# Optimization experiments

Measured on AMD Instinct MI355X. Metric: run time of the kernel, lower is better.

## Reference

```python
import jax, jax.numpy as jnp
import numpy as np

D_MODEL = 1024
N_HEADS = 16
D_K = 64
BATCH = 2
SEQ = 2048
LN_EPS = 1e-5


def setup_inputs() -> dict:
    key = jax.random.key(0)
    ks = jax.random.split(key, 6)
    s = 1.0 / np.sqrt(D_MODEL)
    return {
        "h": jax.random.normal(ks[0], (BATCH, SEQ, D_MODEL), dtype=jnp.float32),
        "Wq": jax.random.normal(ks[1], (D_MODEL, D_MODEL), dtype=jnp.float32) * s,
        "bq": jnp.zeros((D_MODEL,), jnp.float32),
        "Wk": jax.random.normal(ks[2], (D_MODEL, D_MODEL), dtype=jnp.float32) * s,
        "bk": jnp.zeros((D_MODEL,), jnp.float32),
        "Wv": jax.random.normal(ks[3], (D_MODEL, D_MODEL), dtype=jnp.float32) * s,
        "bv": jnp.zeros((D_MODEL,), jnp.float32),
        "Wo": jax.random.normal(ks[4], (D_MODEL, D_MODEL), dtype=jnp.float32) * s,
        "bo": jnp.zeros((D_MODEL,), jnp.float32),
        "ln_w": jnp.ones((D_MODEL,), jnp.float32),
        "ln_b": jnp.zeros((D_MODEL,), jnp.float32),
    }


def _layernorm(x, w, b):
    mu = jnp.mean(x, axis=-1, keepdims=True)
    var = jnp.var(x, axis=-1, keepdims=True)
    return (x - mu) * jax.lax.rsqrt(var + LN_EPS) * w + b


def reference(h, Wq, bq, Wk, bk, Wv, bv, Wo, bo, ln_w, ln_b):
    b, s, _ = h.shape
    scale = 1.0 / np.sqrt(D_K)
    h_res = h
    hn = _layernorm(h, ln_w, ln_b)
    # Linear layers (torch convention: y = x @ W.T + b), split into heads
    q = (hn @ Wq.T + bq).reshape(b, s, N_HEADS, D_K)
    k = (hn @ Wk.T + bk).reshape(b, s, N_HEADS, D_K)
    v = (hn @ Wv.T + bv).reshape(b, s, N_HEADS, D_K)
    attn = jnp.einsum('bihd,bjhd->bhij', q, k) * scale  # [b, h, i, j]
    attn = jax.nn.softmax(attn, axis=-1)
    o = jnp.einsum('bhij,bjhd->bihd', attn, v).reshape(b, s, N_HEADS * D_K)
    out = o @ Wo.T + bo
    return out + h_res
```

## Files before the change

### kernel.cpp

```cpp
#include <hip/hip_runtime.h>
#include <cstdint>

#define D_MODEL 1024
#define N_HEADS 16
#define D_K     64
#define BATCH   2
#define SEQ     2048
#define TOKENS  (BATCH * SEQ)
#define LN_EPS  1e-5f
#define QSCALE  0.18033688011112042f

typedef __bf16 bf16x8 __attribute__((ext_vector_type(8)));
typedef float  floatx4 __attribute__((ext_vector_type(4)));

__device__ __forceinline__ unsigned short f2bf(float f) {
  union { float f; unsigned u; } v; v.f = f;
  unsigned r = v.u + 0x7fffu + ((v.u >> 16) & 1u);
  return (unsigned short)(r >> 16);
}
__device__ __forceinline__ unsigned short f2bf_fast(float f) {
  union { float f; unsigned u; } v; v.f = f;
  return (unsigned short)((v.u + 0x8000u) >> 16);
}

__device__ __forceinline__ void cp16(void* lds, const void* g) {
  __builtin_amdgcn_global_load_lds(
      (__attribute__((address_space(1))) void*)g,
      (__attribute__((address_space(3))) void*)lds, 16, 0, 0);
}

__global__ __launch_bounds__(256) void prep_kernel(
    const float* __restrict__ h, const float* __restrict__ w0,
    const float* __restrict__ w1, const float* __restrict__ w2,
    const float* __restrict__ w3, const float* __restrict__ lw,
    const float* __restrict__ lb, unsigned short* __restrict__ Wcat,
    unsigned short* __restrict__ hn) {
  if (blockIdx.x < 4096) {
    int wsel = blockIdx.x >> 10;
    const float* s = (wsel == 0) ? w0 : (wsel == 1) ? w1 : (wsel == 2) ? w2 : w3;
    unsigned short* d = Wcat + ((size_t)wsel << 20);
    int i = ((blockIdx.x & 1023) << 8) + threadIdx.x;
    float4 v = reinterpret_cast<const float4*>(s)[i];
    ushort4 o;
    o.x = f2bf(v.x); o.y = f2bf(v.y); o.z = f2bf(v.z); o.w = f2bf(v.w);
    reinterpret_cast<ushort4*>(d)[i] = o;
    return;
  }
  int row = blockIdx.x - 4096;
  const float* x = h + (size_t)row * D_MODEL;
  float4 v = reinterpret_cast<const float4*>(x)[threadIdx.x];
  float s  = v.x + v.y + v.z + v.w;
  float s2 = v.x * v.x + v.y * v.y + v.z * v.z + v.w * v.w;
  for (int m = 1; m < 64; m <<= 1) {
    s  += __shfl_xor(s, m);
    s2 += __shfl_xor(s2, m);
  }
  __shared__ float ls[4], ls2[4];
  int wave = threadIdx.x >> 6;
  if ((threadIdx.x & 63) == 0) { ls[wave] = s; ls2[wave] = s2; }
  __syncthreads();
  s  = ls[0] + ls[1] + ls[2] + ls[3];
  s2 = ls2[0] + ls2[1] + ls2[2] + ls2[3];
  float mu  = s * (1.0f / D_MODEL);
  float var = s2 * (1.0f / D_MODEL) - mu * mu;
  float rs  = rsqrtf(var + LN_EPS);
  float4 wv = reinterpret_cast<const float4*>(lw)[threadIdx.x];
  float4 bv = reinterpret_cast<const float4*>(lb)[threadIdx.x];
  ushort4 o;
  o.x = f2bf((v.x - mu) * rs * wv.x + bv.x);
  o.y = f2bf((v.y - mu) * rs * wv.y + bv.y);
  o.z = f2bf((v.z - mu) * rs * wv.z + bv.z);
  o.w = f2bf((v.w - mu) * rs * wv.w + bv.w);
  reinterpret_cast<ushort4*>(hn + (size_t)row * D_MODEL)[threadIdx.x] = o;
}

__global__ __launch_bounds__(256) void gemm_qkv_kernel(
    const unsigned short* __restrict__ A, const unsigned short* __restrict__ Wcat,
    const float* __restrict__ bq, const float* __restrict__ bk,
    const float* __restrict__ bv,
    unsigned short* __restrict__ QK, unsigned short* __restrict__ VtG) {
  __shared__ unsigned short As[128 * 64];
  __shared__ unsigned short Bs[128 * 64];

  const int tid  = threadIdx.x;
  const int w    = tid >> 6;
  const int lane = tid & 63;
  const int l15  = lane & 15;
  const int quad = lane >> 4;
  const int sw   = l15 & 7;
  const int wm = (w >> 1) * 64;
  const int wn = (w & 1) * 64;
  const int bm = blockIdx.y * 128;
  const int bn = blockIdx.x * 128;

  const int srow = tid >> 3;
  const int swzc = (((tid & 7) ^ (srow & 7)) * 8);
  const unsigned short* ga = A    + (size_t)(bm + srow) * 1024 + swzc;
  const unsigned short* gb = Wcat + (size_t)(bn + srow) * 1024 + swzc;
  unsigned short* asl = As + w * 512;
  unsigned short* bsl = Bs + w * 512;

  floatx4 acc[4][4];
  for (int i = 0; i < 4; ++i)
    for (int j = 0; j < 4; ++j) acc[i][j] = {0.f, 0.f, 0.f, 0.f};

  for (int k0 = 0; k0 < 1024; k0 += 64) {
#pragma unroll
    for (int i = 0; i < 4; ++i) cp16(asl + i * 2048, ga + (size_t)i * 32 * 1024 + k0);
#pragma unroll
    for (int i = 0; i < 4; ++i) cp16(bsl + i * 2048, gb + (size_t)i * 32 * 1024 + k0);
    __syncthreads();
#pragma unroll
    for (int kb = 0; kb < 2; ++kb) {
      bf16x8 af[4], bfr[4];
#pragma unroll
      for (int mi = 0; mi < 4; ++mi)
        af[mi] = *reinterpret_cast<const bf16x8*>(
            As + (wm + mi * 16 + l15) * 64 + (((kb * 4 + quad) ^ sw) * 8));
#pragma unroll
      for (int ni = 0; ni < 4; ++ni)
        bfr[ni] = *reinterpret_cast<const bf16x8*>(
            Bs + (wn + ni * 16 + l15) * 64 + (((kb * 4 + quad) ^ sw) * 8));
#pragma unroll
      for (int mi = 0; mi < 4; ++mi)
#pragma unroll
        for (int ni = 0; ni < 4; ++ni)
          acc[mi][ni] = __builtin_amdgcn_mfma_f32_16x16x32_bf16(af[mi], bfr[ni], acc[mi][ni], 0, 0, 0);
    }
    __syncthreads();
  }

  const int wsel = blockIdx.x >> 3;
  if (wsel == 0) {
#pragma unroll
    for (int mi = 0; mi < 4; ++mi)
#pragma unroll
      for (int ni = 0; ni < 4; ++ni) {
        int col = bn + wn + ni * 16 + l15;
        float bb = bq[col];
#pragma unroll
        for (int r = 0; r < 4; ++r) {
          int row = bm + wm + mi * 16 + quad * 4 + r;
          QK[(size_t)row * 2048 + col] = f2bf((acc[mi][ni][r] + bb) * QSCALE);
        }
      }
  } else if (wsel == 1) {
#pragma unroll
    for (int mi = 0; mi < 4; ++mi)
#pragma unroll
      for (int ni = 0; ni < 4; ++ni) {
        int col = bn + wn + ni * 16 + l15;
        float bb = bk[col - 1024];
#pragma unroll
        for (int r = 0; r < 4; ++r) {
          int row = bm + wm + mi * 16 + quad * 4 + r;
          QK[(size_t)row * 2048 + col] = f2bf(acc[mi][ni][r] + bb);
        }
      }
  } else {
#pragma unroll
    for (int mi = 0; mi < 4; ++mi)
#pragma unroll
      for (int ni = 0; ni < 4; ++ni) {
        int d = bn + wn + ni * 16 + l15 - 2048;
        float bb = bv[d];
        ushort4 o;
        o.x = f2bf(acc[mi][ni][0] + bb);
        o.y = f2bf(acc[mi][ni][1] + bb);
        o.z = f2bf(acc[mi][ni][2] + bb);
        o.w = f2bf(acc[mi][ni][3] + bb);
        int row0 = bm + wm + mi * 16 + quad * 4;
        *reinterpret_cast<ushort4*>(VtG + (size_t)d * 4096 + row0) = o;
      }
  }
}

__global__ __launch_bounds__(256) void gemm_out_kernel(
    const unsigned short* __restrict__ A, const unsigned short* __restrict__ Bt,
    const float* __restrict__ bo, const float* __restrict__ resid,
    float* __restrict__ out) {
  __shared__ unsigned short As[128 * 64];
  __shared__ unsigned short Bs[64 * 64];

  const int tid  = threadIdx.x;
  const int w    = tid >> 6;
  const int lane = tid & 63;
  const int l15  = lane & 15;
  const int quad = lane >> 4;
  const int sw   = l15 & 7;
  const int wm = (w >> 1) * 64;
  const int wn = (w & 1) * 32;
  const int bm = blockIdx.y * 128;
  const int bn = blockIdx.x * 64;

  const int srow = tid >> 3;
  const int swzc = (((tid & 7) ^ (srow & 7)) * 8);
  const unsigned short* ga = A  + (size_t)(bm + srow) * 1024 + swzc;
  const unsigned short* gb = Bt + (size_t)(bn + srow) * 1024 + swzc;
  unsigned short* asl = As + w * 512;
  unsigned short* bsl = Bs + w * 512;

  floatx4 acc[4][2];
  for (int i = 0; i < 4; ++i)
    for (int j = 0; j < 2; ++j) acc[i][j] = {0.f, 0.f, 0.f, 0.f};

  for (int k0 = 0; k0 < 1024; k0 += 64) {
#pragma unroll
    for (int i = 0; i < 4; ++i) cp16(asl + i * 2048, ga + (size_t)i * 32 * 1024 + k0);
#pragma unroll
    for (int i = 0; i < 2; ++i) cp16(bsl + i * 2048, gb + (size_t)i * 32 * 1024 + k0);
    __syncthreads();
#pragma unroll
    for (int kb = 0; kb < 2; ++kb) {
      bf16x8 af[4], bfr[2];
#pragma unroll
      for (int mi = 0; mi < 4; ++mi)
        af[mi] = *reinterpret_cast<const bf16x8*>(
            As + (wm + mi * 16 + l15) * 64 + (((kb * 4 + quad) ^ sw) * 8));
#pragma unroll
      for (int ni = 0; ni < 2; ++ni)
        bfr[ni] = *reinterpret_cast<const bf16x8*>(
            Bs + (wn + ni * 16 + l15) * 64 + (((kb * 4 + quad) ^ sw) * 8));
#pragma unroll
      for (int mi = 0; mi < 4; ++mi)
#pragma unroll
        for (int ni = 0; ni < 2; ++ni)
          acc[mi][ni] = __builtin_amdgcn_mfma_f32_16x16x32_bf16(af[mi], bfr[ni], acc[mi][ni], 0, 0, 0);
    }
    __syncthreads();
  }

#pragma unroll
  for (int mi = 0; mi < 4; ++mi)
#pragma unroll
    for (int ni = 0; ni < 2; ++ni) {
      int col = bn + wn + ni * 16 + l15;
      float bb = bo[col];
#pragma unroll
      for (int r = 0; r < 4; ++r) {
        int row = bm + wm + mi * 16 + quad * 4 + r;
        size_t idx = (size_t)row * 1024 + col;
        out[idx] = acc[mi][ni][r] + bb + resid[idx];
      }
    }
}

__global__ __launch_bounds__(256) void attn_kernel(
    const unsigned short* __restrict__ QK, const unsigned short* __restrict__ VtG,
    unsigned short* __restrict__ O) {
  __shared__ unsigned short Ks[128 * 64];
  __shared__ unsigned short Vs[64 * 128];
  __shared__ unsigned short Pl[4 * 32 * 128];

  const int tid  = threadIdx.x;
  const int w    = tid >> 6;
  const int lane = tid & 63;
  const int l15  = lane & 15;
  const int quad = lane >> 4;
  const int sw   = l15 & 7;

  const int hh = blockIdx.x, qt = blockIdx.y, bz = blockIdx.z;
  const int tq0  = bz * SEQ + qt * 128;
  const int hoff = hh * 64;

  bf16x8 qf[2][2];
#pragma unroll
  for (int ms = 0; ms < 2; ++ms) {
    const unsigned short* qp =
        QK + (size_t)(tq0 + w * 32 + ms * 16 + l15) * 2048 + hoff;
    qf[ms][0] = *reinterpret_cast<const bf16x8*>(qp + quad * 8);
    qf[ms][1] = *reinterpret_cast<const bf16x8*>(qp + 32 + quad * 8);
  }

  bf16x8 ones;
#pragma unroll
  for (int j = 0; j < 8; ++j) ones[j] = (__bf16)1.0f;

  floatx4 oacc[2][4], lacc[2];
#pragma unroll
  for (int ms = 0; ms < 2; ++ms) {
    lacc[ms] = {0.f, 0.f, 0.f, 0.f};
#pragma unroll
    for (int d = 0; d < 4; ++d) oacc[ms][d] = {0.f, 0.f, 0.f, 0.f};
  }

  const unsigned short* kg = QK + 1024 + hoff
      + (size_t)(bz * SEQ + (tid >> 3)) * 2048
      + (((tid & 7) ^ ((tid >> 3) & 7)) * 8);
  const unsigned short* vg = VtG
      + (size_t)(hoff + (tid >> 4)) * 4096 + bz * SEQ
      + (((tid & 15) ^ ((tid >> 4) & 7)) * 8);
  unsigned short* ksl = Ks + w * 512;
  unsigned short* vsl = Vs + w * 512;
  unsigned short* wp  = Pl + w * 4096;

  for (int kt = 0; kt < SEQ / 128; ++kt) {
    const unsigned short* kgi = kg + (size_t)(kt * 128) * 2048;
    const unsigned short* vgi = vg + kt * 128;
#pragma unroll
    for (int i = 0; i < 4; ++i) cp16(ksl + i * 2048, kgi + (size_t)(i * 32) * 2048);
#pragma unroll
    for (int i = 0; i < 4; ++i) cp16(vsl + i * 2048, vgi + (size_t)(i * 16) * 4096);
    __syncthreads();

    floatx4 ss[2][8];
#pragma unroll
    for (int ms = 0; ms < 2; ++ms)
#pragma unroll
      for (int nb = 0; nb < 8; ++nb) ss[ms][nb] = {0.f, 0.f, 0.f, 0.f};
#pragma unroll
    for (int nb = 0; nb < 8; ++nb) {
      const unsigned short* krow = Ks + (nb * 16 + l15) * 64;
      bf16x8 kf0 = *reinterpret_cast<const bf16x8*>(krow + ((quad ^ sw) * 8));
      bf16x8 kf1 = *reinterpret_cast<const bf16x8*>(krow + (((4 + quad) ^ sw) * 8));
#pragma unroll
      for (int ms = 0; ms < 2; ++ms) {
        ss[ms][nb] = __builtin_amdgcn_mfma_f32_16x16x32_bf16(kf0, qf[ms][0], ss[ms][nb], 0, 0, 0);
        ss[ms][nb] = __builtin_amdgcn_mfma_f32_16x16x32_bf16(kf1, qf[ms][1], ss[ms][nb], 0, 0, 0);
      }
    }

#pragma unroll
    for (int ms = 0; ms < 2; ++ms)
#pragma unroll
      for (int nb = 0; nb < 8; ++nb) {
        ushort4 pk;
        pk.x = f2bf_fast(__builtin_amdgcn_exp2f(ss[ms][nb][0]));
        pk.y = f2bf_fast(__builtin_amdgcn_exp2f(ss[ms][nb][1]));
        pk.z = f2bf_fast(__builtin_amdgcn_exp2f(ss[ms][nb][2]));
        pk.w = f2bf_fast(__builtin_amdgcn_exp2f(ss[ms][nb][3]));
        int rr = ms * 16 + l15;
        int phys = (nb * 2 + (quad >> 1)) ^ l15;
        *reinterpret_cast<ushort4*>(wp + rr * 128 + phys * 8 + (quad & 1) * 4) = pk;
      }

#pragma unroll
    for (int kf = 0; kf < 4; ++kf) {
      bf16x8 pf[2];
#pragma unroll
      for (int ms = 0; ms < 2; ++ms) {
        int rr = ms * 16 + l15;
        int phys = (kf * 4 + quad) ^ l15;
        pf[ms] = *reinterpret_cast<const bf16x8*>(wp + rr * 128 + phys * 8);
        lacc[ms] = __builtin_amdgcn_mfma_f32_16x16x32_bf16(ones, pf[ms], lacc[ms], 0, 0, 0);
      }
#pragma unroll
      for (int db = 0; db < 4; ++db) {
        bf16x8 vf = *reinterpret_cast<const bf16x8*>(
            Vs + (db * 16 + l15) * 128 + (((kf * 4 + quad) ^ sw) * 8));
#pragma unroll
        for (int ms = 0; ms < 2; ++ms)
          oacc[ms][db] = __builtin_amdgcn_mfma_f32_16x16x32_bf16(vf, pf[ms], oacc[ms][db], 0, 0, 0);
      }
    }
    __syncthreads();
  }

#pragma unroll
  for (int ms = 0; ms < 2; ++ms) {
    float inv = 1.0f / lacc[ms][0];
    unsigned short* ob = O + (size_t)(tq0 + w * 32 + ms * 16 + l15) * 1024
                       + hoff + quad * 4;
#pragma unroll
    for (int db = 0; db < 4; ++db) {
      ushort4 ov;
      ov.x = f2bf_fast(oacc[ms][db][0] * inv);
      ov.y = f2bf_fast(oacc[ms][db][1] * inv);
      ov.z = f2bf_fast(oacc[ms][db][2] * inv);
      ov.w = f2bf_fast(oacc[ms][db][3] * inv);
      *reinterpret_cast<ushort4*>(ob + db * 16) = ov;
    }
  }
}

extern "C" void kernel_launch(void* const* d_in, const int* in_sizes, int n_in,
                              void* d_out, int out_size, void* d_ws, size_t ws_size,
                              hipStream_t stream) {
  const float* h    = (const float*)d_in[0];
  const float* Wq   = (const float*)d_in[1];
  const float* bq   = (const float*)d_in[2];
  const float* Wk   = (const float*)d_in[3];
  const float* bk   = (const float*)d_in[4];
  const float* Wv   = (const float*)d_in[5];
  const float* bv   = (const float*)d_in[6];
  const float* Wo   = (const float*)d_in[7];
  const float* bo   = (const float*)d_in[8];
  const float* ln_w = (const float*)d_in[9];
  const float* ln_b = (const float*)d_in[10];
  float* out = (float*)d_out;

  unsigned short* ws = (unsigned short*)d_ws;
  const size_t WSZ = (size_t)1 << 20;
  unsigned short* Wcat = ws;
  unsigned short* hn   = Wcat + 4 * WSZ;
  unsigned short* QKb  = hn + (size_t)TOKENS * D_MODEL;
  unsigned short* VtG  = QKb + (size_t)TOKENS * 2048;
  unsigned short* Obuf = VtG + (size_t)D_MODEL * TOKENS;

  prep_kernel<<<8192, 256, 0, stream>>>(h, Wq, Wk, Wv, Wo, ln_w, ln_b, Wcat, hn);

  gemm_qkv_kernel<<<dim3(24, 32), 256, 0, stream>>>(hn, Wcat, bq, bk, bv, QKb, VtG);

  attn_kernel<<<dim3(N_HEADS, SEQ / 128, BATCH), 256, 0, stream>>>(QKb, VtG, Obuf);

  gemm_out_kernel<<<dim3(16, 32), 256, 0, stream>>>(Obuf, Wcat + 3 * WSZ, bo, h, out);
}
```

Before: 206.7 us.

## Double-buffer K/V tiles in attention and pack bf16 conversion via perm

Result: faster. 202.0 us (-2.2%).

```diff
diff --git a/kernel.cpp b/kernel.cpp
--- a/kernel.cpp
+++ b/kernel.cpp
@@ -18,9 +18,10 @@
   unsigned r = v.u + 0x7fffu + ((v.u >> 16) & 1u);
   return (unsigned short)(r >> 16);
 }
-__device__ __forceinline__ unsigned short f2bf_fast(float f) {
-  union { float f; unsigned u; } v; v.f = f;
-  return (unsigned short)((v.u + 0x8000u) >> 16);
+__device__ __forceinline__ unsigned pk2bf(float hi, float lo) {
+  union { float f; unsigned u; } a, b;
+  a.f = hi; b.f = lo;
+  return __builtin_amdgcn_perm(a.u, b.u, 0x07060302u);
 }
 
 __device__ __forceinline__ void cp16(void* lds, const void* g) {
@@ -248,9 +249,9 @@
 __global__ __launch_bounds__(256) void attn_kernel(
     const unsigned short* __restrict__ QK, const unsigned short* __restrict__ VtG,
     unsigned short* __restrict__ O) {
-  __shared__ unsigned short Ks[128 * 64];
-  __shared__ unsigned short Vs[64 * 128];
-  __shared__ unsigned short Pl[4 * 32 * 128];
+  __shared__ unsigned short Ks[2][128 * 64];
+  __shared__ unsigned short Vs[2][64 * 128];
+  __shared__ unsigned short Pl[4][32 * 64];
 
   const int tid  = threadIdx.x;
   const int w    = tid >> 6;
@@ -290,18 +291,26 @@
   const unsigned short* vg = VtG
       + (size_t)(hoff + (tid >> 4)) * 4096 + bz * SEQ
       + (((tid & 15) ^ ((tid >> 4) & 7)) * 8);
-  unsigned short* ksl = Ks + w * 512;
-  unsigned short* vsl = Vs + w * 512;
-  unsigned short* wp  = Pl + w * 4096;
-
-  for (int kt = 0; kt < SEQ / 128; ++kt) {
+  unsigned short* wp = Pl[w];
+
+  auto stage = [&](int kt, int b) {
     const unsigned short* kgi = kg + (size_t)(kt * 128) * 2048;
     const unsigned short* vgi = vg + kt * 128;
+    unsigned short* ksl = Ks[b] + w * 512;
+    unsigned short* vsl = Vs[b] + w * 512;
 #pragma unroll
     for (int i = 0; i < 4; ++i) cp16(ksl + i * 2048, kgi + (size_t)(i * 32) * 2048);
 #pragma unroll
     for (int i = 0; i < 4; ++i) cp16(vsl + i * 2048, vgi + (size_t)(i * 16) * 4096);
+  };
+
+  stage(0, 0);
+
+  for (int kt = 0; kt < SEQ / 128; ++kt) {
     __syncthreads();
+    if (kt + 1 < SEQ / 128) stage(kt + 1, (kt + 1) & 1);
+    const unsigned short* Kb = Ks[kt & 1];
+    const unsigned short* Vb = Vs[kt & 1];
 
     floatx4 ss[2][8];
 #pragma unroll
@@ -310,7 +319,7 @@
       for (int nb = 0; nb < 8; ++nb) ss[ms][nb] = {0.f, 0.f, 0.f, 0.f};
 #pragma unroll
     for (int nb = 0; nb < 8; ++nb) {
-      const unsigned short* krow = Ks + (nb * 16 + l15) * 64;
+      const unsigned short* krow = Kb + (nb * 16 + l15) * 64;
       bf16x8 kf0 = *reinterpret_cast<const bf16x8*>(krow + ((quad ^ sw) * 8));
       bf16x8 kf1 = *reinterpret_cast<const bf16x8*>(krow + (((4 + quad) ^ sw) * 8));
 #pragma unroll
@@ -321,39 +330,39 @@
     }
 
 #pragma unroll
-    for (int ms = 0; ms < 2; ++ms)
-#pragma unroll
-      for (int nb = 0; nb < 8; ++nb) {
-        ushort4 pk;
-        pk.x = f2bf_fast(__builtin_amdgcn_exp2f(ss[ms][nb][0]));
-        pk.y = f2bf_fast(__builtin_amdgcn_exp2f(ss[ms][nb][1]));
-        pk.z = f2bf_fast(__builtin_amdgcn_exp2f(ss[ms][nb][2]));
-        pk.w = f2bf_fast(__builtin_amdgcn_exp2f(ss[ms][nb][3]));
-        int rr = ms * 16 + l15;
-        int phys = (nb * 2 + (quad >> 1)) ^ l15;
-        *reinterpret_cast<ushort4*>(wp + rr * 128 + phys * 8 + (quad & 1) * 4) = pk;
-      }
-
-#pragma unroll
-    for (int kf = 0; kf < 4; ++kf) {
-      bf16x8 pf[2];
-#pragma unroll
-      for (int ms = 0; ms < 2; ++ms) {
-        int rr = ms * 16 + l15;
-        int phys = (kf * 4 + quad) ^ l15;
-        pf[ms] = *reinterpret_cast<const bf16x8*>(wp + rr * 128 + phys * 8);
-        lacc[ms] = __builtin_amdgcn_mfma_f32_16x16x32_bf16(ones, pf[ms], lacc[ms], 0, 0, 0);
-      }
-#pragma unroll
-      for (int db = 0; db < 4; ++db) {
-        bf16x8 vf = *reinterpret_cast<const bf16x8*>(
-            Vs + (db * 16 + l15) * 128 + (((kf * 4 + quad) ^ sw) * 8));
-#pragma unroll
-        for (int ms = 0; ms < 2; ++ms)
-          oacc[ms][db] = __builtin_amdgcn_mfma_f32_16x16x32_bf16(vf, pf[ms], oacc[ms][db], 0, 0, 0);
-      }
-    }
-    __syncthreads();
+    for (int c = 0; c < 2; ++c) {
+#pragma unroll
+      for (int ms = 0; ms < 2; ++ms)
+#pragma unroll
+        for (int nb2 = 0; nb2 < 4; ++nb2) {
+          floatx4 sv = ss[ms][c * 4 + nb2];
+          uint2 pk;
+          pk.x = pk2bf(__builtin_amdgcn_exp2f(sv[1]), __builtin_amdgcn_exp2f(sv[0]));
+          pk.y = pk2bf(__builtin_amdgcn_exp2f(sv[3]), __builtin_amdgcn_exp2f(sv[2]));
+          int rr = ms * 16 + l15;
+          int g8 = (nb2 * 2 + (quad >> 1)) ^ sw;
+          *reinterpret_cast<uint2*>(wp + rr * 64 + g8 * 8 + (quad & 1) * 4) = pk;
+        }
+#pragma unroll
+      for (int kf = 0; kf < 2; ++kf) {
+        bf16x8 pf[2];
+#pragma unroll
+        for (int ms = 0; ms < 2; ++ms) {
+          int rr = ms * 16 + l15;
+          int phys = (kf * 4 + quad) ^ sw;
+          pf[ms] = *reinterpret_cast<const bf16x8*>(wp + rr * 64 + phys * 8);
+          lacc[ms] = __builtin_amdgcn_mfma_f32_16x16x32_bf16(ones, pf[ms], lacc[ms], 0, 0, 0);
+        }
+#pragma unroll
+        for (int db = 0; db < 4; ++db) {
+          bf16x8 vf = *reinterpret_cast<const bf16x8*>(
+              Vb + (db * 16 + l15) * 128 + ((((c * 2 + kf) * 4 + quad) ^ sw) * 8));
+#pragma unroll
+          for (int ms = 0; ms < 2; ++ms)
+            oacc[ms][db] = __builtin_amdgcn_mfma_f32_16x16x32_bf16(vf, pf[ms], oacc[ms][db], 0, 0, 0);
+        }
+      }
+    }
   }
 
 #pragma unroll
@@ -363,12 +372,10 @@
                        + hoff + quad * 4;
 #pragma unroll
     for (int db = 0; db < 4; ++db) {
-      ushort4 ov;
-      ov.x = f2bf_fast(oacc[ms][db][0] * inv);
-      ov.y = f2bf_fast(oacc[ms][db][1] * inv);
-      ov.z = f2bf_fast(oacc[ms][db][2] * inv);
-      ov.w = f2bf_fast(oacc[ms][db][3] * inv);
-      *reinterpret_cast<ushort4*>(ob + db * 16) = ov;
+      uint2 ov;
+      ov.x = pk2bf(oacc[ms][db][1] * inv, oacc[ms][db][0] * inv);
+      ov.y = pk2bf(oacc[ms][db][3] * inv, oacc[ms][db][2] * inv);
+      *reinterpret_cast<uint2*>(ob + db * 16) = ov;
     }
   }
 }
```
